# Performance work log

Measured on AMD Instinct MI355X. Metric: run time of the kernel, lower is better.

Reference implementation:

```python
import jax, jax.numpy as jnp
import numpy as np

D_MODEL = 1024
NHEAD = 16
HEAD_DIM = D_MODEL // NHEAD
HID = int(D_MODEL * 4.0 * (2.0 / 3.0))  # 2730, matches int(d_model*mlp_ratio*2/3)
EPS = 1e-5


def setup_inputs() -> dict:
    key = jax.random.key(0)
    ks = jax.random.split(key, 12)
    s = lambda fi, fo: (2.0 / (fi + fo)) ** 0.5
    inp = {
        "x": jax.random.normal(ks[0], (2, 2048, D_MODEL), dtype=jnp.float32),
        "ln1_w": jnp.ones((D_MODEL,), jnp.float32),
        "ln1_b": jnp.zeros((D_MODEL,), jnp.float32),
        "wq": jax.random.normal(ks[1], (D_MODEL, D_MODEL), jnp.float32) * s(D_MODEL, D_MODEL),
        "wk": jax.random.normal(ks[2], (D_MODEL, D_MODEL), jnp.float32) * s(D_MODEL, D_MODEL),
        "wv": jax.random.normal(ks[3], (D_MODEL, D_MODEL), jnp.float32) * s(D_MODEL, D_MODEL),
        "wg": jax.random.normal(ks[4], (D_MODEL, D_MODEL), jnp.float32) * s(D_MODEL, D_MODEL),
        "wo": jax.random.normal(ks[5], (D_MODEL, D_MODEL), jnp.float32) * s(D_MODEL, D_MODEL),
        "ln2_w": jnp.ones((D_MODEL,), jnp.float32),
        "ln2_b": jnp.zeros((D_MODEL,), jnp.float32),
        "w_in": jax.random.normal(ks[6], (D_MODEL, 2 * HID), jnp.float32) * s(D_MODEL, 2 * HID),
        "b_in": jnp.zeros((2 * HID,), jnp.float32),
        "w_out": jax.random.normal(ks[7], (HID, D_MODEL), jnp.float32) * s(HID, D_MODEL),
        "b_out": jnp.zeros((D_MODEL,), jnp.float32),
    }
    return inp


def _layernorm(x, w, b):
    mu = jnp.mean(x, axis=-1, keepdims=True)
    var = jnp.var(x, axis=-1, keepdims=True)
    return (x - mu) * jax.lax.rsqrt(var + EPS) * w + b


def _decay_matrix(S):
    # gamma_h = 1 - 2^{-5-h}, RetNet multiscale decays
    gamma = 1.0 - jnp.exp2(-5.0 - jnp.arange(NHEAD, dtype=jnp.float32))  # [H]
    n = jnp.arange(S, dtype=jnp.float32)
    exp = n[:, None] - n[None, :]                     # [S, S]
    mask = exp >= 0
    d = gamma[:, None, None] ** jnp.where(mask, exp, 0.0)  # [H, S, S]
    return jnp.where(mask[None], d, 0.0)


def _msr(xn, wq, wk, wv, wg, wo):
    B, S, _ = xn.shape
    split = lambda t: t.reshape(B, S, NHEAD, HEAD_DIM).transpose(0, 2, 1, 3)  # bhsd
    q = split(xn @ wq) * (HEAD_DIM ** -0.5)
    k = split(xn @ wk)
    v = split(xn @ wv)
    Dm = _decay_matrix(S)                                   # [H, S, S]
    scores = jnp.einsum("bhsd,bhtd->bhst", q, k) * Dm[None]  # causal decayed retention
    out = jnp.einsum("bhst,bhtd->bhsd", scores, v)
    # per-head normalization (GroupNorm over head dim, no affine)
    mu = jnp.mean(out, axis=-1, keepdims=True)
    var = jnp.var(out, axis=-1, keepdims=True)
    out = (out - mu) * jax.lax.rsqrt(var + 1e-6)
    out = out.transpose(0, 2, 1, 3).reshape(B, S, D_MODEL)
    out = out * jax.nn.silu(xn @ wg)                        # swish gate
    return out @ wo


def _swiglu(x, w_in, b_in, w_out, b_out):
    ab = x @ w_in + b_in
    a, b = ab[..., :HID], ab[..., HID:]
    return (a * jax.nn.silu(b)) @ w_out + b_out


def reference(x, ln1_w, ln1_b, wq, wk, wv, wg, wo, ln2_w, ln2_b, w_in, b_in, w_out, b_out):
    h = _msr(_layernorm(x, ln1_w, ln1_b), wq, wk, wv, wg, wo)
    x = x + h  # dropout/drop_path identity at eval
    x = x + _swiglu(_layernorm(x, ln2_w, ln2_b), w_in, b_in, w_out, b_out)
    return x
```

## Files before the change

### kernel.cpp

```cpp
#include <hip/hip_runtime.h>
#include <math.h>

#define D_MODEL 1024
#define NHEAD   16
#define HDIM    64
#define HID     2730
#define HID_PAD 2816
#define SEQ     2048
#define BATCH   2
#define NTOK    (BATCH * SEQ)
#define QKG     3072

typedef __attribute__((ext_vector_type(8))) short bf16x8;
typedef __attribute__((ext_vector_type(4))) float f32x4;
typedef __attribute__((ext_vector_type(4))) short s16x4;

static __device__ inline short f2bf(float f)
{
    union { float f; unsigned int u; } c; c.f = f;
    unsigned int r = c.u + 0x7FFFu + ((c.u >> 16) & 1u);
    return (short)(r >> 16);
}
static __device__ inline float bf2f(short s)
{
    union { unsigned int u; float f; } c;
    c.u = ((unsigned int)(unsigned short)s) << 16;
    return c.f;
}

#define GLD16(gsrc, ldst) \
    __builtin_amdgcn_global_load_lds((const __attribute__((address_space(1))) void*)(gsrc), \
                                     (__attribute__((address_space(3))) void*)(ldst), 16, 0, 0)


__global__ void ln_kernel(const float* __restrict__ x,
                          const float* __restrict__ w,
                          const float* __restrict__ b,
                          short* __restrict__ out,
                          float eps)
{
    int row = blockIdx.x;
    int t = threadIdx.x;
    const float4* xr = (const float4*)(x + (size_t)row * D_MODEL);
    float4 v = xr[t];
    float s  = v.x + v.y + v.z + v.w;
    float sq = v.x * v.x + v.y * v.y + v.z * v.z + v.w * v.w;
#pragma unroll
    for (int off = 32; off > 0; off >>= 1) {
        s  += __shfl_xor(s, off);
        sq += __shfl_xor(sq, off);
    }
    __shared__ float ss[4], ssq[4];
    int wave = t >> 6;
    if ((t & 63) == 0) { ss[wave] = s; ssq[wave] = sq; }
    __syncthreads();
    s  = ss[0] + ss[1] + ss[2] + ss[3];
    sq = ssq[0] + ssq[1] + ssq[2] + ssq[3];
    float mu  = s * (1.0f / D_MODEL);
    float var = sq * (1.0f / D_MODEL) - mu * mu;
    float inv = rsqrtf(var + eps);
    float4 wv = ((const float4*)w)[t];
    float4 bv = ((const float4*)b)[t];
    s16x4 o;
    o.x = f2bf((v.x - mu) * inv * wv.x + bv.x);
    o.y = f2bf((v.y - mu) * inv * wv.y + bv.y);
    o.z = f2bf((v.z - mu) * inv * wv.z + bv.z);
    o.w = f2bf((v.w - mu) * inv * wv.w + bv.w);
    *(s16x4*)(out + (size_t)row * D_MODEL + 4 * t) = o;
}

struct TJob {
    const float* src;
    short* dst;
    int ldsrc, coloff, nvalid, kvalid, KPAD, NPAD;
};
struct TJobs { TJob j[8]; };

__global__ __launch_bounds__(256) void transpose_all(TJobs jobs)
{
    TJob jb = jobs.j[blockIdx.z];
    int k0 = blockIdx.x * 64, n0 = blockIdx.y * 64;
    if (k0 >= jb.KPAD || n0 >= jb.NPAD) return;
    __shared__ float tile[64][65];
    int t = threadIdx.x;
    {
        int kk = t >> 2, np = (t & 3) << 4;
        int k = k0 + kk;
        bool kok = k < jb.kvalid;
        const float* srow = jb.src + (size_t)k * jb.ldsrc + jb.coloff + n0 + np;
#pragma unroll
        for (int i = 0; i < 16; ++i) {
            int n = n0 + np + i;
            tile[kk][np + i] = (kok && n < jb.nvalid) ? srow[i] : 0.0f;
        }
    }
    __syncthreads();
    {
        int nn = t >> 2, kp = (t & 3) << 4;
        short* drow = jb.dst + (size_t)(n0 + nn) * jb.KPAD + k0 + kp;
#pragma unroll
        for (int v4 = 0; v4 < 4; ++v4) {
            s16x4 o;
            o.x = f2bf(tile[kp + v4 * 4 + 0][nn]);
            o.y = f2bf(tile[kp + v4 * 4 + 1][nn]);
            o.z = f2bf(tile[kp + v4 * 4 + 2][nn]);
            o.w = f2bf(tile[kp + v4 * 4 + 3][nn]);
            *(s16x4*)(drow + v4 * 4) = o;
        }
    }
}

__global__ __launch_bounds__(256, 2) void proj_kernel(
        const short* __restrict__ xn,
        const short* __restrict__ qkgT,
        short* __restrict__ qkg,
        const short* __restrict__ wvT,
        short* __restrict__ vT)
{
    __shared__ short As[2][8192];
    __shared__ short Bs[2][4096];
    const int K = D_MODEL;
    int id = blockIdx.x;
    const short *A, *Bt;
    short* C;
    int ldc, bm, bn;
    if (id < 384) {
        A = xn; Bt = qkgT; C = qkg; ldc = QKG;
        bm = (id & 15) * 256; bn = (id >> 4) * 128;
    } else {
        int i2 = id - 384;
        A = wvT; Bt = xn; C = vT; ldc = NTOK;
        bm = (i2 & 3) * 256; bn = (i2 >> 2) * 128;
    }

    int t = threadIdx.x;
    int w = t >> 6;
    int lane = t & 63;
    int quad = lane >> 4;
    int l15  = lane & 15;
    int x7   = l15 & 7;

    int li3 = lane >> 3;
    int u   = (lane & 7) ^ li3;
    int hi  = u >> 2;
    int qk  = (u & 3) << 3;
    const short* gA = A + (size_t)(bm + hi * 128 + w * 32 + li3) * K + qk;
    const short* gB = Bt + (size_t)(bn + hi * 64 + w * 16 + li3) * K + qk;

    int abase = l15 * 64 + ((((w >> 1) << 2) | quad) ^ x7) * 8;
    int bbase = l15 * 64 + ((((w & 1) << 2) | quad) ^ x7) * 8;

    f32x4 acc[8][4];
#pragma unroll
    for (int i = 0; i < 8; ++i)
#pragma unroll
        for (int j = 0; j < 4; ++j) acc[i][j] = (f32x4){0.f, 0.f, 0.f, 0.f};

#pragma unroll
    for (int c = 0; c < 4; ++c)
        GLD16(gA + (size_t)c * 8 * K, &As[0][w * 2048 + c * 512]);
#pragma unroll
    for (int c = 0; c < 2; ++c)
        GLD16(gB + (size_t)c * 8 * K, &Bs[0][w * 1024 + c * 512]);

    for (int k0 = 0; k0 < K; k0 += 32) {
        int cur = (k0 >> 5) & 1;
        __syncthreads();
        int k1 = k0 + 32;
        if (k1 < K) {
#pragma unroll
            for (int c = 0; c < 4; ++c)
                GLD16(gA + (size_t)c * 8 * K + k1, &As[cur ^ 1][w * 2048 + c * 512]);
#pragma unroll
            for (int c = 0; c < 2; ++c)
                GLD16(gB + (size_t)c * 8 * K + k1, &Bs[cur ^ 1][w * 1024 + c * 512]);
        }
        bf16x8 af[8], bfr[4];
#pragma unroll
        for (int m = 0; m < 8; ++m)
            af[m] = *(const bf16x8*)(&As[cur][m * 1024 + abase]);
#pragma unroll
        for (int jf = 0; jf < 4; ++jf)
            bfr[jf] = *(const bf16x8*)(&Bs[cur][jf * 1024 + bbase]);
#pragma unroll
        for (int m = 0; m < 8; ++m)
#pragma unroll
            for (int jf = 0; jf < 4; ++jf)
                acc[m][jf] = __builtin_amdgcn_mfma_f32_16x16x32_bf16(af[m], bfr[jf], acc[m][jf], 0, 0, 0);
    }

#pragma unroll
    for (int m = 0; m < 8; ++m) {
        int gr = bm + (w >> 1) * 128 + m * 16 + quad * 4;
#pragma unroll
        for (int jf = 0; jf < 4; ++jf) {
            int gc = bn + (w & 1) * 64 + jf * 16 + l15;
#pragma unroll
            for (int r = 0; r < 4; ++r)
                C[(size_t)(gr + r) * ldc + gc] = f2bf(acc[m][jf][r]);
        }
    }
}

template<int EPI>
__global__ __launch_bounds__(256, 4) void gemm_n64(
        const short* __restrict__ A, int lda,
        const short* __restrict__ Bt,
        const float* __restrict__ bias,
        const float* __restrict__ R, int ldr,
        void* __restrict__ C, int ldc, int K)
{
    __shared__ short As[2][4096];
    __shared__ short Bs[2][2048];
    int bm = blockIdx.x * 128;
    int bn = blockIdx.y * 64;
    int t = threadIdx.x;
    int w = t >> 6;
    int lane = t & 63;
    int quad = lane >> 4;
    int l15  = lane & 15;
    int x7   = l15 & 7;

    int p0 = t >> 3;
    int u  = (t & 7) ^ (p0 & 7);
    int scol = (u & 3) << 3;
    const short* gA0 = A  + (size_t)(bm + p0 + ((u >> 2) << 6)) * lda + scol;
    const short* gA1 = gA0 + (size_t)32 * lda;
    const short* gB0 = Bt + (size_t)(bn + p0 + ((u >> 2) << 5)) * K + scol;
    int wb = w << 9;

    int wr = (w >> 1) * 64;
    int wc = (w & 1) * 32;
    int aoff = l15 * 64 + (((((w >> 1) << 2) | quad) ^ x7) << 3);
    int boff = l15 * 64 + (((((w & 1) << 2) | quad) ^ x7) << 3);

    f32x4 acc[4][2];
#pragma unroll
    for (int i = 0; i < 4; ++i)
#pragma unroll
        for (int j = 0; j < 2; ++j) acc[i][j] = (f32x4){0.f, 0.f, 0.f, 0.f};

    GLD16(gA0, &As[0][wb]);
    GLD16(gA1, &As[0][2048 + wb]);
    GLD16(gB0, &Bs[0][wb]);

    for (int k0 = 0; k0 < K; k0 += 32) {
        int cur = (k0 >> 5) & 1;
        __syncthreads();
        int k1 = k0 + 32;
        if (k1 < K) {
            GLD16(gA0 + k1, &As[cur ^ 1][wb]);
            GLD16(gA1 + k1, &As[cur ^ 1][2048 + wb]);
            GLD16(gB0 + k1, &Bs[cur ^ 1][wb]);
        }
        bf16x8 af[4], bfr[2];
#pragma unroll
        for (int i = 0; i < 4; ++i)
            af[i] = *(const bf16x8*)(&As[cur][i * 1024 + aoff]);
#pragma unroll
        for (int j = 0; j < 2; ++j)
            bfr[j] = *(const bf16x8*)(&Bs[cur][j * 1024 + boff]);
#pragma unroll
        for (int i = 0; i < 4; ++i)
#pragma unroll
            for (int j = 0; j < 2; ++j)
                acc[i][j] = __builtin_amdgcn_mfma_f32_16x16x32_bf16(af[i], bfr[j], acc[i][j], 0, 0, 0);
    }

#pragma unroll
    for (int i = 0; i < 4; ++i) {
        int gr = bm + wr + i * 16 + quad * 4;
#pragma unroll
        for (int j = 0; j < 2; ++j) {
            int gc = bn + wc + j * 16 + l15;
#pragma unroll
            for (int r = 0; r < 4; ++r) {
                float val = acc[i][j][r];
                size_t idx = (size_t)(gr + r) * ldc + gc;
                if (EPI == 0) {
                    ((short*)C)[idx] = f2bf(val);
                } else if (EPI == 1) {
                    ((float*)C)[idx] = val + R[(size_t)(gr + r) * ldr + gc];
                } else {
                    ((float*)C)[idx] = val + bias[gc] + R[(size_t)(gr + r) * ldr + gc];
                }
            }
        }
    }
}

__global__ __launch_bounds__(256, 2) void mlp_fused(
        const short* __restrict__ A,
        const short* __restrict__ w_inT,
        const float* __restrict__ b_in,
        short* __restrict__ hm)
{
    __shared__ short As[2][8192];
    __shared__ short Bs[2][4096];
    const int K = D_MODEL;
    int bm = blockIdx.y * 256;
    int bn = blockIdx.x * 64;
    int t = threadIdx.x;
    int w = t >> 6;
    int lane = t & 63;
    int quad = lane >> 4;
    int l15  = lane & 15;
    int x7   = l15 & 7;

    int li3 = lane >> 3;
    int u   = (lane & 7) ^ li3;
    int hi  = u >> 2;
    int qk  = (u & 3) << 3;
    const short* gA = A + (size_t)(bm + hi * 128 + w * 32 + li3) * K + qk;
    int f = hi * 4 + w;
    const short* gB = w_inT + (size_t)(((f & 1) ? HID_PAD : 0) + bn
                                       + ((f >> 1) << 4) + li3) * K + qk;

    int abase = l15 * 64 + ((((w >> 1) << 2) | quad) ^ x7) * 8;
    int bbase = l15 * 64 + ((((w & 1) << 2) | quad) ^ x7) * 8;

    f32x4 acc[8][4];
#pragma unroll
    for (int i = 0; i < 8; ++i)
#pragma unroll
        for (int j = 0; j < 4; ++j) acc[i][j] = (f32x4){0.f, 0.f, 0.f, 0.f};

#pragma unroll
    for (int c = 0; c < 4; ++c)
        GLD16(gA + (size_t)c * 8 * K, &As[0][w * 2048 + c * 512]);
#pragma unroll
    for (int c = 0; c < 2; ++c)
        GLD16(gB + (size_t)c * 8 * K, &Bs[0][w * 1024 + c * 512]);

    for (int k0 = 0; k0 < K; k0 += 32) {
        int cur = (k0 >> 5) & 1;
        __syncthreads();
        int k1 = k0 + 32;
        if (k1 < K) {
#pragma unroll
            for (int c = 0; c < 4; ++c)
                GLD16(gA + (size_t)c * 8 * K + k1, &As[cur ^ 1][w * 2048 + c * 512]);
#pragma unroll
            for (int c = 0; c < 2; ++c)
                GLD16(gB + (size_t)c * 8 * K + k1, &Bs[cur ^ 1][w * 1024 + c * 512]);
        }
        bf16x8 af[8], bfr[4];
#pragma unroll
        for (int m = 0; m < 8; ++m)
            af[m] = *(const bf16x8*)(&As[cur][m * 1024 + abase]);
#pragma unroll
        for (int jf = 0; jf < 4; ++jf)
            bfr[jf] = *(const bf16x8*)(&Bs[cur][jf * 1024 + bbase]);
#pragma unroll
        for (int m = 0; m < 8; ++m)
#pragma unroll
            for (int jf = 0; jf < 4; ++jf)
                acc[m][jf] = __builtin_amdgcn_mfma_f32_16x16x32_bf16(af[m], bfr[jf], acc[m][jf], 0, 0, 0);
    }

#pragma unroll
    for (int m = 0; m < 8; ++m) {
        int gr = bm + (w >> 1) * 128 + m * 16 + quad * 4;
#pragma unroll
        for (int jj = 0; jj < 2; ++jj) {
            int gc = bn + (((w & 1) << 1) + jj) * 16 + l15;
            bool ok = gc < HID;
            float ba = ok ? b_in[gc] : 0.0f;
            float bb = ok ? b_in[HID + gc] : 0.0f;
#pragma unroll
            for (int r = 0; r < 4; ++r) {
                float a  = acc[m][2 * jj][r] + ba;
                float bv = acc[m][2 * jj + 1][r] + bb;
                float val = ok ? a * (bv / (1.0f + expf(-bv))) : 0.0f;
                hm[(size_t)(gr + r) * HID_PAD + gc] = f2bf(val);
            }
        }
    }
}

#define PSTR 72

__global__ __launch_bounds__(512) void retention_mfma(
        const short* __restrict__ qkg,
        const short* __restrict__ vT,
        short* __restrict__ rg)
{
    int i  = blockIdx.x;
    int xg = i & 15;
    int h  = (i >> 4) & 15;
    int b  = i >> 8;
    int qb = b ? xg : 15 - xg;

    __shared__ short ks[2][4096];
    __shared__ short vt[2][4096];
    __shared__ short ps[8][16 * PSTR];

    int tid  = threadIdx.x;
    int w    = tid >> 6;
    int lane = tid & 63;
    int quad = lane >> 4;
    int l15  = lane & 15;
    int x7   = l15 & 7;

    float log2g = log1pf(-exp2f(-5.0f - (float)h)) * 1.4426950408889634f;
    int hcol = h * HDIM;
    int s0 = qb * 128;
    size_t tok0 = (size_t)b * SEQ;

    int sch  = tid >> 8;
    int p0r  = (tid >> 3) & 31;
    int ur   = (tid & 7) ^ (p0r & 7);
    int srw  = p0r + ((ur >> 2) << 5);
    int sc8  = (ur & 3) << 3;
    const short* kbase  = qkg + (tok0 + srw) * QKG + 1024 + hcol + sch * 32 + sc8;
    const short* vtbase = vT + (size_t)(hcol + srw) * NTOK + tok0 + sch * 32 + sc8;
    int lb = tid << 3;

    const short* qrow = qkg + (tok0 + s0 + w * 16 + l15) * QKG + hcol;
    bf16x8 qa0 = *(const bf16x8*)(qrow + quad * 8);
    bf16x8 qa1 = *(const bf16x8*)(qrow + 32 + quad * 8);

    float colfac[4];
#pragma unroll
    for (int tile = 0; tile < 4; ++tile)
        colfac[tile] = exp2f(-(float)(tile * 16 + l15) * log2g) * 0.125f;

    f32x4 oacc[4];
#pragma unroll
    for (int k = 0; k < 4; ++k) oacc[k] = (f32x4){0.f, 0.f, 0.f, 0.f};

    int sbase = s0 + w * 16 + quad * 4;
    int tmax = 2 * qb + 1;

    GLD16(kbase, &ks[0][lb]);
    GLD16(vtbase, &vt[0][lb]);

    for (int tb = 0; tb <= tmax; ++tb) {
        int cur = tb & 1;
        __syncthreads();
        if (tb < tmax) {
            GLD16(kbase + (size_t)(tb + 1) * 64 * QKG, &ks[cur ^ 1][lb]);
            GLD16(vtbase + (tb + 1) * 64, &vt[cur ^ 1][lb]);
        }

        f32x4 sacc[4];
#pragma unroll
        for (int k = 0; k < 4; ++k) sacc[k] = (f32x4){0.f, 0.f, 0.f, 0.f};
#pragma unroll
        for (int tile = 0; tile < 4; ++tile) {
            int kaddr = ((tile & 1) * 16 + l15) * 64 +
                        (((((tile >> 1) << 2) | quad) ^ x7) << 3);
            bf16x8 kb0 = *(const bf16x8*)(&ks[cur][kaddr]);
            bf16x8 kb1 = *(const bf16x8*)(&ks[cur][2048 + kaddr]);
            sacc[tile] = __builtin_amdgcn_mfma_f32_16x16x32_bf16(qa0, kb0, sacc[tile], 0, 0, 0);
            sacc[tile] = __builtin_amdgcn_mfma_f32_16x16x32_bf16(qa1, kb1, sacc[tile], 0, 0, 0);
        }

        int fbi = sbase - tb * 64;
        float rf[4];
#pragma unroll
        for (int reg = 0; reg < 4; ++reg)
            rf[reg] = exp2f((float)(fbi + reg) * log2g);

        if (tb * 64 + 63 > s0 + w * 16) {
#pragma unroll
            for (int tile = 0; tile < 4; ++tile) {
                int tt = tile * 16 + l15;
#pragma unroll
                for (int reg = 0; reg < 4; ++reg) {
                    float p = (fbi + reg >= tt) ? sacc[tile][reg] * rf[reg] * colfac[tile] : 0.0f;
                    ps[w][(quad * 4 + reg) * PSTR + tile * 16 + l15] = f2bf(p);
                }
            }
        } else {
#pragma unroll
            for (int tile = 0; tile < 4; ++tile)
#pragma unroll
                for (int reg = 0; reg < 4; ++reg)
                    ps[w][(quad * 4 + reg) * PSTR + tile * 16 + l15] =
                        f2bf(sacc[tile][reg] * (rf[reg] * colfac[tile]));
        }

#pragma unroll
        for (int ksi = 0; ksi < 2; ++ksi) {
            bf16x8 pa = *(const bf16x8*)(&ps[w][l15 * PSTR + ksi * 32 + quad * 8]);
#pragma unroll
            for (int dt = 0; dt < 4; ++dt) {
                int vaddr = ((dt & 1) * 16 + l15) * 64 +
                            (((((dt >> 1) << 2) | quad) ^ x7) << 3);
                bf16x8 vb = *(const bf16x8*)(&vt[cur][ksi * 2048 + vaddr]);
                oacc[dt] = __builtin_amdgcn_mfma_f32_16x16x32_bf16(pa, vb, oacc[dt], 0, 0, 0);
            }
        }
    }

    float s1[4], s2[4];
#pragma unroll
    for (int reg = 0; reg < 4; ++reg) {
        s1[reg] = oacc[0][reg] + oacc[1][reg] + oacc[2][reg] + oacc[3][reg];
        s2[reg] = oacc[0][reg] * oacc[0][reg] + oacc[1][reg] * oacc[1][reg]
                + oacc[2][reg] * oacc[2][reg] + oacc[3][reg] * oacc[3][reg];
    }
#pragma unroll
    for (int off = 1; off < 16; off <<= 1) {
#pragma unroll
        for (int reg = 0; reg < 4; ++reg) {
            s1[reg] += __shfl_xor(s1[reg], off);
            s2[reg] += __shfl_xor(s2[reg], off);
        }
    }
    size_t rowtok = tok0 + s0 + w * 16 + quad * 4;
    short* obase = rg + rowtok * D_MODEL + hcol;
    const short* gbase = qkg + rowtok * QKG + 2048 + hcol;
#pragma unroll
    for (int reg = 0; reg < 4; ++reg) {
        float mu  = s1[reg] * (1.0f / 64.0f);
        float var = s2[reg] * (1.0f / 64.0f) - mu * mu;
        float inv = rsqrtf(var + 1e-6f);
#pragma unroll
        for (int dt = 0; dt < 4; ++dt) {
            float gv = bf2f(gbase[(size_t)reg * QKG + dt * 16 + l15]);
            float val = (oacc[dt][reg] - mu) * inv * (gv / (1.0f + expf(-gv)));
            obase[(size_t)reg * D_MODEL + dt * 16 + l15] = f2bf(val);
        }
    }
}

extern "C" void kernel_launch(void* const* d_in, const int* in_sizes, int n_in,
                              void* d_out, int out_size, void* d_ws, size_t ws_size,
                              hipStream_t stream)
{
    const float* x     = (const float*)d_in[0];
    const float* ln1w  = (const float*)d_in[1];
    const float* ln1b  = (const float*)d_in[2];
    const float* wq    = (const float*)d_in[3];
    const float* wk    = (const float*)d_in[4];
    const float* wv    = (const float*)d_in[5];
    const float* wg    = (const float*)d_in[6];
    const float* wo    = (const float*)d_in[7];
    const float* ln2w  = (const float*)d_in[8];
    const float* ln2b  = (const float*)d_in[9];
    const float* w_in  = (const float*)d_in[10];
    const float* b_in  = (const float*)d_in[11];
    const float* w_out = (const float*)d_in[12];
    const float* b_out = (const float*)d_in[13];
    float* out = (float*)d_out;
    char* base = (char*)d_ws;

    const size_t MB = 1u << 20;
    short* xn     = (short*)(base);
    short* qkgT   = (short*)(base +  8 * MB);
    short* wvT    = (short*)(base + 14 * MB);
    short* woT    = (short*)(base + 16 * MB);
    short* w_inT  = (short*)(base + 18 * MB);
    short* w_outT = (short*)(base + 29 * MB);
    short* qkg    = (short*)(base + 35 * MB);
    short* hm     = (short*)(base + 35 * MB);
    short* vT     = (short*)(base + 59 * MB);
    short* rg     = (short*)(base + 67 * MB);

    TJobs jobs;
    jobs.j[0] = { wq,    qkgT,                          1024,    0, 1024, 1024, 1024, 1024 };
    jobs.j[1] = { wk,    qkgT + 1024 * 1024,            1024,    0, 1024, 1024, 1024, 1024 };
    jobs.j[2] = { wg,    qkgT + 2 * 1024 * 1024,        1024,    0, 1024, 1024, 1024, 1024 };
    jobs.j[3] = { wv,    wvT,                           1024,    0, 1024, 1024, 1024, 1024 };
    jobs.j[4] = { wo,    woT,                           1024,    0, 1024, 1024, 1024, 1024 };
    jobs.j[5] = { w_in,  w_inT,                         2 * HID, 0,   HID, 1024, 1024, HID_PAD };
    jobs.j[6] = { w_in,  w_inT + (size_t)HID_PAD * 1024, 2 * HID, HID, HID, 1024, 1024, HID_PAD };
    jobs.j[7] = { w_out, w_outT,                        1024,    0, 1024, HID, HID_PAD, 1024 };
    transpose_all<<<dim3(44, 44, 8), 256, 0, stream>>>(jobs);

    ln_kernel<<<NTOK, 256, 0, stream>>>(x, ln1w, ln1b, xn, 1e-5f);
    proj_kernel<<<512, 256, 0, stream>>>(xn, qkgT, qkg, wvT, vT);
    retention_mfma<<<512, 512, 0, stream>>>(qkg, vT, rg);
    gemm_n64<1><<<dim3(32, 16), 256, 0, stream>>>(rg, D_MODEL, woT, nullptr, x, D_MODEL, out, D_MODEL, D_MODEL);
    ln_kernel<<<NTOK, 256, 0, stream>>>(out, ln2w, ln2b, xn, 1e-5f);
    mlp_fused<<<dim3(HID_PAD / 64, NTOK / 256), 256, 0, stream>>>(xn, w_inT, b_in, hm);
    gemm_n64<2><<<dim3(32, 16), 256, 0, stream>>>(hm, HID_PAD, w_outT, b_out, out, D_MODEL, out, D_MODEL, HID_PAD);
}
```

Measured before the change: 394.5 us.

## Merge LN1 with weight transposes, swap MLP grid order, incrementalize decay factors

LayerNorm-1 and all weight transposes now run as one launch with a compact block list, replacing a padded 44x44x8 grid in which many blocks exit immediately, and removing one launch. The MLP grid axes are swapped so consecutive blocks walk the M dimension while sharing the same weight columns, which may improve cache reuse. In the retention loop, the per-tile row decay exp2f calls are replaced by a running multiply by a fixed step factor. That multiply can accumulate rounding error or underflow over long sequences.

```diff
diff --git a/kernel.cpp b/kernel.cpp
--- a/kernel.cpp
+++ b/kernel.cpp
@@ -76,13 +76,68 @@
 };
 struct TJobs { TJob j[8]; };
 
-__global__ __launch_bounds__(256) void transpose_all(TJobs jobs)
-{
-    TJob jb = jobs.j[blockIdx.z];
-    int k0 = blockIdx.x * 64, n0 = blockIdx.y * 64;
-    if (k0 >= jb.KPAD || n0 >= jb.NPAD) return;
+#define TRN_BLOCKS 3392
+
+__global__ __launch_bounds__(256) void prep_kernel(
+        const float* __restrict__ x,
+        const float* __restrict__ ln1w,
+        const float* __restrict__ ln1b,
+        short* __restrict__ xn,
+        TJobs jobs)
+{
     __shared__ float tile[64][65];
+    __shared__ float ss[4], ssq[4];
+    int bid = blockIdx.x;
     int t = threadIdx.x;
+
+    if (bid < NTOK) {
+        int row = bid;
+        const float4* xr = (const float4*)(x + (size_t)row * D_MODEL);
+        float4 v = xr[t];
+        float s  = v.x + v.y + v.z + v.w;
+        float sq = v.x * v.x + v.y * v.y + v.z * v.z + v.w * v.w;
+#pragma unroll
+        for (int off = 32; off > 0; off >>= 1) {
+            s  += __shfl_xor(s, off);
+            sq += __shfl_xor(sq, off);
+        }
+        int wave = t >> 6;
+        if ((t & 63) == 0) { ss[wave] = s; ssq[wave] = sq; }
+        __syncthreads();
+        s  = ss[0] + ss[1] + ss[2] + ss[3];
+        sq = ssq[0] + ssq[1] + ssq[2] + ssq[3];
+        float mu  = s * (1.0f / D_MODEL);
+        float var = sq * (1.0f / D_MODEL) - mu * mu;
+        float inv = rsqrtf(var + 1e-5f);
+        float4 wv = ((const float4*)ln1w)[t];
+        float4 bv = ((const float4*)ln1b)[t];
+        s16x4 o;
+        o.x = f2bf((v.x - mu) * inv * wv.x + bv.x);
+        o.y = f2bf((v.y - mu) * inv * wv.y + bv.y);
+        o.z = f2bf((v.z - mu) * inv * wv.z + bv.z);
+        o.w = f2bf((v.w - mu) * inv * wv.w + bv.w);
+        *(s16x4*)(xn + (size_t)row * D_MODEL + 4 * t) = o;
+        return;
+    }
+
+    int local = bid - NTOK;
+    int jbi, kt, nt;
+    if (local < 1280) {
+        jbi = local >> 8;
+        int l = local & 255;
+        kt = l & 15; nt = l >> 4;
+    } else if (local < 2688) {
+        int l2 = local - 1280;
+        jbi = 5 + (l2 >= 704 ? 1 : 0);
+        int l3 = (l2 >= 704) ? l2 - 704 : l2;
+        kt = l3 & 15; nt = l3 >> 4;
+    } else {
+        int l4 = local - 2688;
+        jbi = 7;
+        kt = l4 % 44; nt = l4 / 44;
+    }
+    TJob jb = jobs.j[jbi];
+    int k0 = kt * 64, n0 = nt * 64;
     {
         int kk = t >> 2, np = (t & 3) << 4;
         int k = k0 + kk;
@@ -298,8 +353,8 @@
     __shared__ short As[2][8192];
     __shared__ short Bs[2][4096];
     const int K = D_MODEL;
-    int bm = blockIdx.y * 256;
-    int bn = blockIdx.x * 64;
+    int bm = blockIdx.x * 256;
+    int bn = blockIdx.y * 64;
     int t = threadIdx.x;
     int w = t >> 6;
     int lane = t & 63;
@@ -432,6 +487,12 @@
     int sbase = s0 + w * 16 + quad * 4;
     int tmax = 2 * qb + 1;
 
+    float rf[4];
+#pragma unroll
+    for (int reg = 0; reg < 4; ++reg)
+        rf[reg] = exp2f((float)(sbase + reg) * log2g);
+    float gstep = exp2f(-64.0f * log2g);
+
     GLD16(kbase, &ks[0][lb]);
     GLD16(vtbase, &vt[0][lb]);
 
@@ -457,10 +518,6 @@
         }
 
         int fbi = sbase - tb * 64;
-        float rf[4];
-#pragma unroll
-        for (int reg = 0; reg < 4; ++reg)
-            rf[reg] = exp2f((float)(fbi + reg) * log2g);
 
         if (tb * 64 + 63 > s0 + w * 16) {
 #pragma unroll
@@ -480,6 +537,9 @@
                     ps[w][(quad * 4 + reg) * PSTR + tile * 16 + l15] =
                         f2bf(sacc[tile][reg] * (rf[reg] * colfac[tile]));
         }
+#pragma unroll
+        for (int reg = 0; reg < 4; ++reg)
+            rf[reg] *= gstep;
 
 #pragma unroll
         for (int ksi = 0; ksi < 2; ++ksi) {
@@ -568,13 +628,12 @@
     jobs.j[5] = { w_in,  w_inT,                         2 * HID, 0,   HID, 1024, 1024, HID_PAD };
     jobs.j[6] = { w_in,  w_inT + (size_t)HID_PAD * 1024, 2 * HID, HID, HID, 1024, 1024, HID_PAD };
     jobs.j[7] = { w_out, w_outT,                        1024,    0, 1024, HID, HID_PAD, 1024 };
-    transpose_all<<<dim3(44, 44, 8), 256, 0, stream>>>(jobs);
-
-    ln_kernel<<<NTOK, 256, 0, stream>>>(x, ln1w, ln1b, xn, 1e-5f);
+
+    prep_kernel<<<NTOK + TRN_BLOCKS, 256, 0, stream>>>(x, ln1w, ln1b, xn, jobs);
     proj_kernel<<<512, 256, 0, stream>>>(xn, qkgT, qkg, wvT, vT);
     retention_mfma<<<512, 512, 0, stream>>>(qkg, vT, rg);
     gemm_n64<1><<<dim3(32, 16), 256, 0, stream>>>(rg, D_MODEL, woT, nullptr, x, D_MODEL, out, D_MODEL, D_MODEL);
     ln_kernel<<<NTOK, 256, 0, stream>>>(out, ln2w, ln2b, xn, 1e-5f);
-    mlp_fused<<<dim3(HID_PAD / 64, NTOK / 256), 256, 0, stream>>>(xn, w_inT, b_in, hm);
+    mlp_fused<<<dim3(NTOK / 256, HID_PAD / 64), 256, 0, stream>>>(xn, w_inT, b_in, hm);
     gemm_n64<2><<<dim3(32, 16), 256, 0, stream>>>(hm, HID_PAD, w_outT, b_out, out, D_MODEL, out, D_MODEL, HID_PAD);
 }
```

After: 375.3 us. 4.9% less time.
